# Kernel optimization log

Hardware: AMD Instinct MI355X
Metric: run time of the kernel (lower is better)

The kernel has to match this reference:

```python
import jax, jax.numpy as jnp
import numpy as np

N = 50000
E = 400000
IN_C, HID, OUT2, NCLS = 128, 512, 64, 2
NEG_SLOPE = 0.2


def setup_inputs() -> dict:
    key = jax.random.key(0)
    ks = jax.random.split(key, 12)
    x = jax.random.normal(ks[0], (N, IN_C), dtype=jnp.float32)
    edge_index = jax.random.randint(ks[1], (2, E), 0, N, dtype=jnp.int64)
    def glorot(k, shape):
        fan_in = shape[0]
        return jax.random.normal(k, shape, dtype=jnp.float32) / np.float32(np.sqrt(fan_in))
    return {
        "x": x,
        "edge_index": edge_index,
        "W1": glorot(ks[2], (IN_C, HID)),
        "a1_src": glorot(ks[3], (HID,)),
        "a1_dst": glorot(ks[4], (HID,)),
        "b1": jnp.zeros((HID,), jnp.float32),
        "W2": glorot(ks[5], (HID, OUT2)),
        "a2_src": glorot(ks[6], (OUT2,)),
        "a2_dst": glorot(ks[7], (OUT2,)),
        "b2": jnp.zeros((OUT2,), jnp.float32),
        "fcW": glorot(ks[8], (OUT2, NCLS)),
        "fcb": jnp.zeros((NCLS,), jnp.float32),
    }


def _gat_conv(h_in, src, dst, W, a_src, a_dst, b):
    # single-head GATConv (PyG defaults: heads=1, negative_slope=0.2, self-loops already added)
    h = h_in @ W                                   # [N, D]
    alpha_s = h @ a_src                            # [N]
    alpha_d = h @ a_dst                            # [N]
    e = jax.nn.leaky_relu(alpha_s[src] + alpha_d[dst], NEG_SLOPE)  # [E']
    # segment softmax over incoming edges of each dst node
    m = jax.ops.segment_max(e, dst, num_segments=N)
    ex = jnp.exp(e - m[dst])
    denom = jax.ops.segment_sum(ex, dst, num_segments=N)
    alpha = ex / denom[dst]                        # [E']
    out = jax.ops.segment_sum(alpha[:, None] * h[src], dst, num_segments=N)
    return out + b


def reference(x, edge_index, W1, a1_src, a1_dst, b1, W2, a2_src, a2_dst, b2, fcW, fcb):
    loops = jnp.arange(N, dtype=edge_index.dtype)
    src = jnp.concatenate([edge_index[0], loops])  # add self loops (PyG default)
    dst = jnp.concatenate([edge_index[1], loops])
    h = jax.nn.relu(_gat_conv(x, src, dst, W1, a1_src, a1_dst, b1))
    h = jax.nn.relu(_gat_conv(h, src, dst, W2, a2_src, a2_dst, b2))
    # F.dropout(training=self.training): identity in eval mode
    return h @ fcW + fcb
```

## Files before the change

kernel.cpp:

```cpp
#include <hip/hip_runtime.h>

#define N_NODES 50000
#define N_EDGES 400000
#define E_TOT   (N_EDGES + N_NODES)
#define IN_C 128
#define HID  512
#define OUT2 64
#define NEG_SLOPE 0.2f

typedef short bf16x8 __attribute__((ext_vector_type(8)));
typedef float f32x4  __attribute__((ext_vector_type(4)));

__device__ __forceinline__ float wave_sum(float v) {
#pragma unroll
  for (int o = 32; o > 0; o >>= 1) v += __shfl_xor(v, o, 64);
  return v;
}
__device__ __forceinline__ int wave_sum_i(int v) {
#pragma unroll
  for (int o = 32; o > 0; o >>= 1) v += __shfl_xor(v, o, 64);
  return v;
}
__device__ __forceinline__ float wave_max(float v) {
#pragma unroll
  for (int o = 32; o > 0; o >>= 1) v = fmaxf(v, __shfl_xor(v, o, 64));
  return v;
}
__device__ __forceinline__ float leaky(float t) {
  return (t > 0.f) ? t : NEG_SLOPE * t;
}

__device__ __forceinline__ unsigned short bf16_rne(float x) {
  unsigned u = __float_as_uint(x);
  u += 0x7fffu + ((u >> 16) & 1u);
  return (unsigned short)(u >> 16);
}
__device__ __forceinline__ void split_bf16(float x, unsigned short& h, unsigned short& l) {
  h = bf16_rne(x);
  float hf = __uint_as_float(((unsigned)h) << 16);
  l = bf16_rne(x - hf);
}

__device__ __forceinline__ int esrc(const int* __restrict__ ei, int e) {
  return (e < N_EDGES) ? ei[e] : (e - N_EDGES);
}
__device__ __forceinline__ int edst(const int* __restrict__ ei, int e) {
  return (e < N_EDGES) ? ei[N_EDGES + e] : (e - N_EDGES);
}

__global__ void count_deg(const int* __restrict__ ei, int* __restrict__ deg) {
  int e = blockIdx.x * blockDim.x + threadIdx.x;
  if (e >= E_TOT) return;
  atomicAdd(&deg[edst(ei, e)], 1);
}

__global__ void scanA(const int* __restrict__ deg, int* __restrict__ bsum) {
  __shared__ int ws[16];
  int t = threadIdx.x, lane = t & 63, w = t >> 6;
  int i = blockIdx.x * 1024 + t;
  int v = (i < N_NODES) ? deg[i] : 0;
  int s = wave_sum_i(v);
  if (lane == 0) ws[w] = s;
  __syncthreads();
  if (t == 0) {
    int tot = 0;
#pragma unroll
    for (int k = 0; k < 16; k++) tot += ws[k];
    bsum[blockIdx.x] = tot;
  }
}

__global__ void scanB(const int* __restrict__ bsum, int* __restrict__ boff, int nb) {
  int lane = threadIdx.x;
  int v = (lane < nb) ? bsum[lane] : 0;
  int sc = v;
#pragma unroll
  for (int off = 1; off < 64; off <<= 1) {
    int u = __shfl_up(sc, off, 64);
    if (lane >= off) sc += u;
  }
  if (lane < nb) boff[lane] = sc - v;
}

__global__ void scanC(const int* __restrict__ deg, const int* __restrict__ boff,
                      int* __restrict__ row_ptr) {
  __shared__ int ws[16];
  int t = threadIdx.x, lane = t & 63, w = t >> 6;
  int i = blockIdx.x * 1024 + t;
  int v = (i < N_NODES) ? deg[i] : 0;
  int sc = v;
#pragma unroll
  for (int off = 1; off < 64; off <<= 1) {
    int u = __shfl_up(sc, off, 64);
    if (lane >= off) sc += u;
  }
  if (lane == 63) ws[w] = sc;
  __syncthreads();
  if (w == 0 && lane < 16) {
    int u = ws[lane];
#pragma unroll
    for (int off = 1; off < 16; off <<= 1) {
      int uu = __shfl_up(u, off, 64);
      if (lane >= off) u += uu;
    }
    ws[lane] = u;
  }
  __syncthreads();
  int excl = ((w > 0) ? ws[w - 1] : 0) + boff[blockIdx.x];
  if (i < N_NODES) row_ptr[i + 1] = sc + excl;
  if (blockIdx.x == 0 && t == 0) row_ptr[0] = 0;
}

__global__ void fill_csr(const int* __restrict__ ei, const int* __restrict__ row_ptr,
                         int* __restrict__ cursor, int* __restrict__ csr_src) {
  int e = blockIdx.x * blockDim.x + threadIdx.x;
  if (e >= E_TOT) return;
  int d = edst(ei, e);
  int pos = atomicAdd(&cursor[d], 1);
  csr_src[row_ptr[d] + pos] = esrc(ei, e);
}

__global__ void prep_w1_frag(const float* __restrict__ W1, unsigned short* __restrict__ W1F) {
  int t = blockIdx.x * 256 + threadIdx.x;
  if (t >= 128 * 64) return;
  int fi = t >> 6, l = t & 63;
  int ks = fi & 3, n = (fi >> 2) & 3, jt = fi >> 4;
  int col = jt * 64 + n * 16 + (l & 15);
  int k0 = ks * 32 + (l >> 4) * 8;
  unsigned short hv[8], lv[8];
#pragma unroll
  for (int e = 0; e < 8; e++)
    split_bf16(W1[(size_t)(k0 + e) * HID + col], hv[e], lv[e]);
  unsigned short* ph = W1F + ((size_t)(fi * 2 + 0) * 64 + l) * 8;
  unsigned short* pl = W1F + ((size_t)(fi * 2 + 1) * 64 + l) * 8;
#pragma unroll
  for (int e = 0; e < 8; e++) { ph[e] = hv[e]; pl[e] = lv[e]; }
}

__global__ void prep_w2_frag(const float* __restrict__ W2, unsigned short* __restrict__ W2F) {
  int t = blockIdx.x * 256 + threadIdx.x;
  if (t >= 64 * 64) return;
  int fi = t >> 6, l = t & 63;
  int n = fi & 3, ks = (fi >> 2) & 1, jt = fi >> 3;
  int col = n * 16 + (l & 15);
  int k0 = jt * 64 + ks * 32 + (l >> 4) * 8;
  unsigned short hv[8], lv[8];
#pragma unroll
  for (int e = 0; e < 8; e++)
    split_bf16(W2[(size_t)(k0 + e) * OUT2 + col], hv[e], lv[e]);
  unsigned short* ph = W2F + ((size_t)(fi * 2 + 0) * 64 + l) * 8;
  unsigned short* pl = W2F + ((size_t)(fi * 2 + 1) * 64 + l) * 8;
#pragma unroll
  for (int e = 0; e < 8; e++) { ph[e] = hv[e]; pl[e] = lv[e]; }
}

__global__ void matvec_w1(const float* __restrict__ W1, const float* __restrict__ a1s,
                          const float* __restrict__ a1d, float* __restrict__ w1s,
                          float* __restrict__ w1d) {
  int wid = (blockIdx.x * blockDim.x + threadIdx.x) >> 6;
  int lane = threadIdx.x & 63;
  if (wid >= IN_C) return;
  const float* row = W1 + (size_t)wid * HID;
  float s = 0.f, d = 0.f;
#pragma unroll
  for (int j0 = 0; j0 < HID; j0 += 64) {
    float w = row[j0 + lane];
    s += w * a1s[j0 + lane];
    d += w * a1d[j0 + lane];
  }
  s = wave_sum(s); d = wave_sum(d);
  if (lane == 0) { w1s[wid] = s; w1d[wid] = d; }
}

__global__ void node_scores128(const float* __restrict__ x, const float* __restrict__ ws,
                               const float* __restrict__ wd, float* __restrict__ as_,
                               float* __restrict__ ad_) {
  int wid = (blockIdx.x * blockDim.x + threadIdx.x) >> 6;
  int lane = threadIdx.x & 63;
  if (wid >= N_NODES) return;
  float2 v = ((const float2*)(x + (size_t)wid * IN_C))[lane];
  float2 w1 = ((const float2*)ws)[lane];
  float2 w2 = ((const float2*)wd)[lane];
  float s = wave_sum(v.x * w1.x + v.y * w1.y);
  float d = wave_sum(v.x * w2.x + v.y * w2.y);
  if (lane == 0) { as_[wid] = s; ad_[wid] = d; }
}

__global__ void sm_agg1(const int* __restrict__ row_ptr, const int* __restrict__ csr_src,
                        const float* __restrict__ as_, const float* __restrict__ ad_,
                        const float* __restrict__ x, float* __restrict__ xa) {
  int wid = (blockIdx.x * blockDim.x + threadIdx.x) >> 6;
  int lane = threadIdx.x & 63;
  if (wid >= N_NODES) return;
  int beg = row_ptr[wid], end = row_ptr[wid + 1];
  int deg = end - beg;
  float adv = ad_[wid];
  const float2* x2 = (const float2*)x;
  float2 acc = make_float2(0.f, 0.f);
  if (deg <= 64) {
    int s = 0; float sc = -3.4e38f;
    if (lane < deg) { s = csr_src[beg + lane]; sc = leaky(as_[s] + adv); }
    float m = wave_max(sc);
    float ex = (lane < deg) ? __expf(sc - m) : 0.f;
    float sum = wave_sum(ex);
    float a = ex / sum;
    int kk = 0;
    for (; kk + 4 <= deg; kk += 4) {
      float w0 = __shfl(a, kk, 64),     w1 = __shfl(a, kk + 1, 64);
      float w2 = __shfl(a, kk + 2, 64), w3 = __shfl(a, kk + 3, 64);
      int s0 = __shfl(s, kk, 64),     s1 = __shfl(s, kk + 1, 64);
      int s2 = __shfl(s, kk + 2, 64), s3 = __shfl(s, kk + 3, 64);
      float2 r0 = x2[(size_t)s0 * 64 + lane];
      float2 r1 = x2[(size_t)s1 * 64 + lane];
      float2 r2 = x2[(size_t)s2 * 64 + lane];
      float2 r3 = x2[(size_t)s3 * 64 + lane];
      acc.x += w0 * r0.x + w1 * r1.x + w2 * r2.x + w3 * r3.x;
      acc.y += w0 * r0.y + w1 * r1.y + w2 * r2.y + w3 * r3.y;
    }
    for (; kk < deg; kk++) {
      float w = __shfl(a, kk, 64);
      int sv = __shfl(s, kk, 64);
      float2 r = x2[(size_t)sv * 64 + lane];
      acc.x += w * r.x; acc.y += w * r.y;
    }
  } else {
    float m = -3.4e38f;
    for (int k = beg + lane; k < end; k += 64)
      m = fmaxf(m, leaky(as_[csr_src[k]] + adv));
    m = wave_max(m);
    float sum = 0.f;
    for (int k = beg + lane; k < end; k += 64)
      sum += __expf(leaky(as_[csr_src[k]] + adv) - m);
    sum = wave_sum(sum);
    float inv = 1.f / sum;
    for (int k = beg; k < end; k++) {
      int sv = csr_src[k];
      float w = __expf(leaky(as_[sv] + adv) - m) * inv;
      float2 r = x2[(size_t)sv * 64 + lane];
      acc.x += w * r.x; acc.y += w * r.y;
    }
  }
  ((float2*)(xa + (size_t)wid * IN_C))[lane] = acc;
}

__launch_bounds__(128, 2)
__global__ void fused_gemm_mfma(const float* __restrict__ xa,
                                const unsigned short* __restrict__ W1F,
                                const float* __restrict__ b1,
                                const unsigned short* __restrict__ W2F,
                                const float* __restrict__ a2s, const float* __restrict__ a2d,
                                float* __restrict__ h2, float* __restrict__ as2,
                                float* __restrict__ ad2) {
  __shared__ unsigned int TS[64][64];
  int t = threadIdx.x;
  int w = t >> 6;
  int l = t & 63;
  int lr = l & 15;
  int G  = l >> 4;
  int base = blockIdx.x * 64 + w * 32;

  bf16x8 aFh[2][4], aFl[2][4];
#pragma unroll
  for (int m = 0; m < 2; m++) {
    int grow = base + m * 16 + lr;
    bool ok = (grow < N_NODES);
    const float* rp = xa + (size_t)grow * IN_C;
#pragma unroll
    for (int ks = 0; ks < 4; ks++) {
      float4 v0 = make_float4(0.f, 0.f, 0.f, 0.f), v1 = v0;
      if (ok) {
        v0 = *(const float4*)(rp + ks * 32 + G * 8);
        v1 = *(const float4*)(rp + ks * 32 + G * 8 + 4);
      }
      unsigned short h, lo;
      split_bf16(v0.x, h, lo); aFh[m][ks][0] = (short)h; aFl[m][ks][0] = (short)lo;
      split_bf16(v0.y, h, lo); aFh[m][ks][1] = (short)h; aFl[m][ks][1] = (short)lo;
      split_bf16(v0.z, h, lo); aFh[m][ks][2] = (short)h; aFl[m][ks][2] = (short)lo;
      split_bf16(v0.w, h, lo); aFh[m][ks][3] = (short)h; aFl[m][ks][3] = (short)lo;
      split_bf16(v1.x, h, lo); aFh[m][ks][4] = (short)h; aFl[m][ks][4] = (short)lo;
      split_bf16(v1.y, h, lo); aFh[m][ks][5] = (short)h; aFl[m][ks][5] = (short)lo;
      split_bf16(v1.z, h, lo); aFh[m][ks][6] = (short)h; aFl[m][ks][6] = (short)lo;
      split_bf16(v1.w, h, lo); aFh[m][ks][7] = (short)h; aFl[m][ks][7] = (short)lo;
    }
  }

  const bf16x8* W1Fv = (const bf16x8*)W1F;
  const bf16x8* W2Fv = (const bf16x8*)W2F;

  f32x4 acc2[2][4];
#pragma unroll
  for (int m = 0; m < 2; m++)
#pragma unroll
    for (int n = 0; n < 4; n++) acc2[m][n] = (f32x4){0.f, 0.f, 0.f, 0.f};

  for (int jt = 0; jt < 8; jt++) {
    f32x4 acc1[2][4];
#pragma unroll
    for (int m = 0; m < 2; m++)
#pragma unroll
      for (int n = 0; n < 4; n++) acc1[m][n] = (f32x4){0.f, 0.f, 0.f, 0.f};
#pragma unroll
    for (int ks = 0; ks < 4; ks++) {
#pragma unroll
      for (int n = 0; n < 4; n++) {
        int fi = (jt * 4 + n) * 4 + ks;
        bf16x8 b_h = W1Fv[(size_t)(fi * 2 + 0) * 64 + l];
        bf16x8 b_l = W1Fv[(size_t)(fi * 2 + 1) * 64 + l];
#pragma unroll
        for (int m = 0; m < 2; m++) {
          acc1[m][n] = __builtin_amdgcn_mfma_f32_16x16x32_bf16(aFh[m][ks], b_h, acc1[m][n], 0, 0, 0);
          acc1[m][n] = __builtin_amdgcn_mfma_f32_16x16x32_bf16(aFl[m][ks], b_h, acc1[m][n], 0, 0, 0);
          acc1[m][n] = __builtin_amdgcn_mfma_f32_16x16x32_bf16(aFh[m][ks], b_l, acc1[m][n], 0, 0, 0);
        }
      }
    }
#pragma unroll
    for (int n = 0; n < 4; n++) {
      float bv = b1[jt * 64 + n * 16 + lr];
#pragma unroll
      for (int m = 0; m < 2; m++) {
#pragma unroll
        for (int r = 0; r < 4; r++) {
          float vv = fmaxf(acc1[m][n][r] + bv, 0.f);
          unsigned short hh, ll;
          split_bf16(vv, hh, ll);
          int rowL = w * 32 + m * 16 + G * 4 + r;
          int colS = (n * 16 + lr) ^ ((rowL & 7) << 2);
          TS[rowL][colS] = (unsigned)hh | ((unsigned)ll << 16);
        }
      }
    }
#pragma unroll
    for (int ks = 0; ks < 2; ks++) {
      int kl = ks * 32 + G * 8;
      bf16x8 a2h[2], a2l[2];
#pragma unroll
      for (int m = 0; m < 2; m++) {
        int rowA = w * 32 + m * 16 + lr;
        int sw2 = (rowA & 7) << 2;
        uint4 q0 = *(const uint4*)&TS[rowA][(kl + 0) ^ sw2];
        uint4 q1 = *(const uint4*)&TS[rowA][(kl + 4) ^ sw2];
        a2h[m][0] = (short)(q0.x & 0xffff); a2l[m][0] = (short)(q0.x >> 16);
        a2h[m][1] = (short)(q0.y & 0xffff); a2l[m][1] = (short)(q0.y >> 16);
        a2h[m][2] = (short)(q0.z & 0xffff); a2l[m][2] = (short)(q0.z >> 16);
        a2h[m][3] = (short)(q0.w & 0xffff); a2l[m][3] = (short)(q0.w >> 16);
        a2h[m][4] = (short)(q1.x & 0xffff); a2l[m][4] = (short)(q1.x >> 16);
        a2h[m][5] = (short)(q1.y & 0xffff); a2l[m][5] = (short)(q1.y >> 16);
        a2h[m][6] = (short)(q1.z & 0xffff); a2l[m][6] = (short)(q1.z >> 16);
        a2h[m][7] = (short)(q1.w & 0xffff); a2l[m][7] = (short)(q1.w >> 16);
      }
#pragma unroll
      for (int n = 0; n < 4; n++) {
        int fi2 = (jt * 2 + ks) * 4 + n;
        bf16x8 b_h = W2Fv[(size_t)(fi2 * 2 + 0) * 64 + l];
        bf16x8 b_l = W2Fv[(size_t)(fi2 * 2 + 1) * 64 + l];
#pragma unroll
        for (int m = 0; m < 2; m++) {
          acc2[m][n] = __builtin_amdgcn_mfma_f32_16x16x32_bf16(a2h[m], b_h, acc2[m][n], 0, 0, 0);
          acc2[m][n] = __builtin_amdgcn_mfma_f32_16x16x32_bf16(a2l[m], b_h, acc2[m][n], 0, 0, 0);
          acc2[m][n] = __builtin_amdgcn_mfma_f32_16x16x32_bf16(a2h[m], b_l, acc2[m][n], 0, 0, 0);
        }
      }
    }
  }

#pragma unroll
  for (int m = 0; m < 2; m++) {
#pragma unroll
    for (int r = 0; r < 4; r++) {
      int grow = base + m * 16 + G * 4 + r;
      if (grow < N_NODES) {
#pragma unroll
        for (int n = 0; n < 4; n++)
          h2[(size_t)grow * OUT2 + n * 16 + lr] = acc2[m][n][r];
      }
      float sp = 0.f, dp = 0.f;
#pragma unroll
      for (int n = 0; n < 4; n++) {
        float v = acc2[m][n][r];
        sp += v * a2s[n * 16 + lr];
        dp += v * a2d[n * 16 + lr];
      }
#pragma unroll
      for (int o = 1; o < 16; o <<= 1) {
        sp += __shfl_xor(sp, o, 64);
        dp += __shfl_xor(dp, o, 64);
      }
      if (lr == 0 && grow < N_NODES) { as2[grow] = sp; ad2[grow] = dp; }
    }
  }
}

__global__ void sm_agg2_final(const int* __restrict__ row_ptr, const int* __restrict__ csr_src,
                              const float* __restrict__ as_, const float* __restrict__ ad_,
                              const float* __restrict__ h2, const float* __restrict__ b2,
                              const float* __restrict__ fcW, const float* __restrict__ fcb,
                              float* __restrict__ out) {
  int wid = (blockIdx.x * blockDim.x + threadIdx.x) >> 6;
  int lane = threadIdx.x & 63;
  if (wid >= N_NODES) return;
  int beg = row_ptr[wid], end = row_ptr[wid + 1];
  int deg = end - beg;
  float adv = ad_[wid];
  float acc = 0.f;
  if (deg <= 64) {
    int s = 0; float sc = -3.4e38f;
    if (lane < deg) { s = csr_src[beg + lane]; sc = leaky(as_[s] + adv); }
    float m = wave_max(sc);
    float ex = (lane < deg) ? __expf(sc - m) : 0.f;
    float sum = wave_sum(ex);
    float a = ex / sum;
    int kk = 0;
    for (; kk + 4 <= deg; kk += 4) {
      float w0 = __shfl(a, kk, 64),     w1 = __shfl(a, kk + 1, 64);
      float w2 = __shfl(a, kk + 2, 64), w3 = __shfl(a, kk + 3, 64);
      int s0 = __shfl(s, kk, 64),     s1 = __shfl(s, kk + 1, 64);
      int s2 = __shfl(s, kk + 2, 64), s3 = __shfl(s, kk + 3, 64);
      float r0 = h2[(size_t)s0 * OUT2 + lane];
      float r1 = h2[(size_t)s1 * OUT2 + lane];
      float r2 = h2[(size_t)s2 * OUT2 + lane];
      float r3 = h2[(size_t)s3 * OUT2 + lane];
      acc += w0 * r0 + w1 * r1 + w2 * r2 + w3 * r3;
    }
    for (; kk < deg; kk++) {
      float w = __shfl(a, kk, 64);
      int sv = __shfl(s, kk, 64);
      acc += w * h2[(size_t)sv * OUT2 + lane];
    }
  } else {
    float m = -3.4e38f;
    for (int k = beg + lane; k < end; k += 64)
      m = fmaxf(m, leaky(as_[csr_src[k]] + adv));
    m = wave_max(m);
    float sum = 0.f;
    for (int k = beg + lane; k < end; k += 64)
      sum += __expf(leaky(as_[csr_src[k]] + adv) - m);
    sum = wave_sum(sum);
    float inv = 1.f / sum;
    for (int k = beg; k < end; k++) {
      int sv = csr_src[k];
      float w = __expf(leaky(as_[sv] + adv) - m) * inv;
      acc += w * h2[(size_t)sv * OUT2 + lane];
    }
  }
  float v = fmaxf(acc + b2[lane], 0.f);
  float2 fw = ((const float2*)fcW)[lane];
  float f0 = wave_sum(v * fw.x);
  float f1 = wave_sum(v * fw.y);
  if (lane == 0) {
    out[(size_t)wid * 2 + 0] = f0 + fcb[0];
    out[(size_t)wid * 2 + 1] = f1 + fcb[1];
  }
}

extern "C" void kernel_launch(void* const* d_in, const int* in_sizes, int n_in,
                              void* d_out, int out_size, void* d_ws, size_t ws_size,
                              hipStream_t stream) {
  const float* x    = (const float*)d_in[0];
  const int*   ei   = (const int*)d_in[1];
  const float* W1   = (const float*)d_in[2];
  const float* a1s  = (const float*)d_in[3];
  const float* a1d  = (const float*)d_in[4];
  const float* b1   = (const float*)d_in[5];
  const float* W2   = (const float*)d_in[6];
  const float* a2s  = (const float*)d_in[7];
  const float* a2d  = (const float*)d_in[8];
  const float* b2   = (const float*)d_in[9];
  const float* fcW  = (const float*)d_in[10];
  const float* fcb  = (const float*)d_in[11];
  float* out = (float*)d_out;

  char* p = (char*)d_ws;
  float* xa    = (float*)p; p += (size_t)N_NODES * IN_C * 4;
  float* h2    = (float*)p; p += (size_t)N_NODES * OUT2 * 4;
  float* as1   = (float*)p; p += (size_t)N_NODES * 4;
  float* ad1   = (float*)p; p += (size_t)N_NODES * 4;
  float* w1s   = (float*)p; p += 256 * 4;
  float* w1d   = (float*)p; p += 256 * 4;
  int* row_ptr = (int*)p;   p += (size_t)(N_NODES + 4) * 4;
  int* deg     = (int*)p;   p += (size_t)N_NODES * 4;
  int* bsum    = (int*)p;   p += 64 * 4;
  int* boff    = (int*)p;   p += 64 * 4;
  int* csr_src = (int*)p;   p += (size_t)E_TOT * 4;
  unsigned short* W1F = (unsigned short*)p; p += (size_t)128 * 2 * 64 * 8 * 2;
  unsigned short* W2F = (unsigned short*)p; p += (size_t)64 * 2 * 64 * 8 * 2;

  const int edge_blocks = (E_TOT + 255) / 256;
  const int node_wave_blocks = (N_NODES + 3) / 4;
  const int m_tiles64 = (N_NODES + 63) / 64;
  const int scan_blocks = (N_NODES + 1023) / 1024;

  hipMemsetAsync(deg, 0, (size_t)N_NODES * 4, stream);
  count_deg<<<edge_blocks, 256, 0, stream>>>(ei, deg);
  scanA<<<scan_blocks, 1024, 0, stream>>>(deg, bsum);
  scanB<<<1, 64, 0, stream>>>(bsum, boff, scan_blocks);
  scanC<<<scan_blocks, 1024, 0, stream>>>(deg, boff, row_ptr);
  hipMemsetAsync(deg, 0, (size_t)N_NODES * 4, stream);
  fill_csr<<<edge_blocks, 256, 0, stream>>>(ei, row_ptr, deg, csr_src);
  prep_w1_frag<<<(128 * 64 + 255) / 256, 256, 0, stream>>>(W1, W1F);
  prep_w2_frag<<<(64 * 64 + 255) / 256, 256, 0, stream>>>(W2, W2F);

  matvec_w1<<<(IN_C + 3) / 4, 256, 0, stream>>>(W1, a1s, a1d, w1s, w1d);
  node_scores128<<<node_wave_blocks, 256, 0, stream>>>(x, w1s, w1d, as1, ad1);
  sm_agg1<<<node_wave_blocks, 256, 0, stream>>>(row_ptr, csr_src, as1, ad1, x, xa);

  fused_gemm_mfma<<<m_tiles64, 128, 0, stream>>>(xa, W1F, b1, W2F,
                                                 a2s, a2d, h2, as1, ad1);

  sm_agg2_final<<<node_wave_blocks, 256, 0, stream>>>(row_ptr, csr_src, as1, ad1, h2, b2,
                                                      fcW, fcb, out);
}
```

Measured before the change: 272.9 us.

## Merge weight prep kernels, unroll gather loops by 8, hoist MFMA B-fragment loads

Three weight-preparation kernels (W1 fragment split, W2 fragment split, W1·a matvec) are folded into one launch to cut launch overhead. The gather-aggregate loops in both softmax-aggregation kernels gain an 8-wide unrolled stage, so more independent row loads are in flight per wave. In the fused MFMA GEMM, the W1 and W2 fragment loads are batched ahead of the MFMA chains to expose memory-level parallelism. In exchange, register pressure rises, which could lower occupancy.

```diff
diff --git a/kernel.cpp b/kernel.cpp
--- a/kernel.cpp
+++ b/kernel.cpp
@@ -120,56 +120,54 @@
   csr_src[row_ptr[d] + pos] = esrc(ei, e);
 }
 
-__global__ void prep_w1_frag(const float* __restrict__ W1, unsigned short* __restrict__ W1F) {
-  int t = blockIdx.x * 256 + threadIdx.x;
-  if (t >= 128 * 64) return;
-  int fi = t >> 6, l = t & 63;
-  int ks = fi & 3, n = (fi >> 2) & 3, jt = fi >> 4;
-  int col = jt * 64 + n * 16 + (l & 15);
-  int k0 = ks * 32 + (l >> 4) * 8;
-  unsigned short hv[8], lv[8];
-#pragma unroll
-  for (int e = 0; e < 8; e++)
-    split_bf16(W1[(size_t)(k0 + e) * HID + col], hv[e], lv[e]);
-  unsigned short* ph = W1F + ((size_t)(fi * 2 + 0) * 64 + l) * 8;
-  unsigned short* pl = W1F + ((size_t)(fi * 2 + 1) * 64 + l) * 8;
-#pragma unroll
-  for (int e = 0; e < 8; e++) { ph[e] = hv[e]; pl[e] = lv[e]; }
-}
-
-__global__ void prep_w2_frag(const float* __restrict__ W2, unsigned short* __restrict__ W2F) {
-  int t = blockIdx.x * 256 + threadIdx.x;
-  if (t >= 64 * 64) return;
-  int fi = t >> 6, l = t & 63;
-  int n = fi & 3, ks = (fi >> 2) & 1, jt = fi >> 3;
-  int col = n * 16 + (l & 15);
-  int k0 = jt * 64 + ks * 32 + (l >> 4) * 8;
-  unsigned short hv[8], lv[8];
-#pragma unroll
-  for (int e = 0; e < 8; e++)
-    split_bf16(W2[(size_t)(k0 + e) * OUT2 + col], hv[e], lv[e]);
-  unsigned short* ph = W2F + ((size_t)(fi * 2 + 0) * 64 + l) * 8;
-  unsigned short* pl = W2F + ((size_t)(fi * 2 + 1) * 64 + l) * 8;
-#pragma unroll
-  for (int e = 0; e < 8; e++) { ph[e] = hv[e]; pl[e] = lv[e]; }
-}
-
-__global__ void matvec_w1(const float* __restrict__ W1, const float* __restrict__ a1s,
-                          const float* __restrict__ a1d, float* __restrict__ w1s,
-                          float* __restrict__ w1d) {
-  int wid = (blockIdx.x * blockDim.x + threadIdx.x) >> 6;
-  int lane = threadIdx.x & 63;
-  if (wid >= IN_C) return;
-  const float* row = W1 + (size_t)wid * HID;
-  float s = 0.f, d = 0.f;
-#pragma unroll
-  for (int j0 = 0; j0 < HID; j0 += 64) {
-    float w = row[j0 + lane];
-    s += w * a1s[j0 + lane];
-    d += w * a1d[j0 + lane];
-  }
-  s = wave_sum(s); d = wave_sum(d);
-  if (lane == 0) { w1s[wid] = s; w1d[wid] = d; }
+__global__ void prep_weights(const float* __restrict__ W1, const float* __restrict__ W2,
+                             const float* __restrict__ a1s, const float* __restrict__ a1d,
+                             unsigned short* __restrict__ W1F, unsigned short* __restrict__ W2F,
+                             float* __restrict__ w1s, float* __restrict__ w1d) {
+  int b = blockIdx.x;
+  if (b < 32) {
+    int t = b * 256 + threadIdx.x;
+    int fi = t >> 6, l = t & 63;
+    int ks = fi & 3, n = (fi >> 2) & 3, jt = fi >> 4;
+    int col = jt * 64 + n * 16 + (l & 15);
+    int k0 = ks * 32 + (l >> 4) * 8;
+    unsigned short hv[8], lv[8];
+#pragma unroll
+    for (int e = 0; e < 8; e++)
+      split_bf16(W1[(size_t)(k0 + e) * HID + col], hv[e], lv[e]);
+    unsigned short* ph = W1F + ((size_t)(fi * 2 + 0) * 64 + l) * 8;
+    unsigned short* pl = W1F + ((size_t)(fi * 2 + 1) * 64 + l) * 8;
+#pragma unroll
+    for (int e = 0; e < 8; e++) { ph[e] = hv[e]; pl[e] = lv[e]; }
+  } else if (b < 48) {
+    int t = (b - 32) * 256 + threadIdx.x;
+    int fi = t >> 6, l = t & 63;
+    int n = fi & 3, ks = (fi >> 2) & 1, jt = fi >> 3;
+    int col = n * 16 + (l & 15);
+    int k0 = jt * 64 + ks * 32 + (l >> 4) * 8;
+    unsigned short hv[8], lv[8];
+#pragma unroll
+    for (int e = 0; e < 8; e++)
+      split_bf16(W2[(size_t)(k0 + e) * OUT2 + col], hv[e], lv[e]);
+    unsigned short* ph = W2F + ((size_t)(fi * 2 + 0) * 64 + l) * 8;
+    unsigned short* pl = W2F + ((size_t)(fi * 2 + 1) * 64 + l) * 8;
+#pragma unroll
+    for (int e = 0; e < 8; e++) { ph[e] = hv[e]; pl[e] = lv[e]; }
+  } else {
+    int wid = ((b - 48) * 256 + threadIdx.x) >> 6;
+    int lane = threadIdx.x & 63;
+    if (wid >= IN_C) return;
+    const float* row = W1 + (size_t)wid * HID;
+    float s = 0.f, d = 0.f;
+#pragma unroll
+    for (int j0 = 0; j0 < HID; j0 += 64) {
+      float w = row[j0 + lane];
+      s += w * a1s[j0 + lane];
+      d += w * a1d[j0 + lane];
+    }
+    s = wave_sum(s); d = wave_sum(d);
+    if (lane == 0) { w1s[wid] = s; w1d[wid] = d; }
+  }
 }
 
 __global__ void node_scores128(const float* __restrict__ x, const float* __restrict__ ws,
@@ -205,6 +203,28 @@
     float sum = wave_sum(ex);
     float a = ex / sum;
     int kk = 0;
+    for (; kk + 8 <= deg; kk += 8) {
+      float w0 = __shfl(a, kk, 64),     w1 = __shfl(a, kk + 1, 64);
+      float w2 = __shfl(a, kk + 2, 64), w3 = __shfl(a, kk + 3, 64);
+      float w4 = __shfl(a, kk + 4, 64), w5 = __shfl(a, kk + 5, 64);
+      float w6 = __shfl(a, kk + 6, 64), w7 = __shfl(a, kk + 7, 64);
+      int s0 = __shfl(s, kk, 64),     s1 = __shfl(s, kk + 1, 64);
+      int s2 = __shfl(s, kk + 2, 64), s3 = __shfl(s, kk + 3, 64);
+      int s4 = __shfl(s, kk + 4, 64), s5 = __shfl(s, kk + 5, 64);
+      int s6 = __shfl(s, kk + 6, 64), s7 = __shfl(s, kk + 7, 64);
+      float2 r0 = x2[(size_t)s0 * 64 + lane];
+      float2 r1 = x2[(size_t)s1 * 64 + lane];
+      float2 r2 = x2[(size_t)s2 * 64 + lane];
+      float2 r3 = x2[(size_t)s3 * 64 + lane];
+      float2 r4 = x2[(size_t)s4 * 64 + lane];
+      float2 r5 = x2[(size_t)s5 * 64 + lane];
+      float2 r6 = x2[(size_t)s6 * 64 + lane];
+      float2 r7 = x2[(size_t)s7 * 64 + lane];
+      acc.x += w0 * r0.x + w1 * r1.x + w2 * r2.x + w3 * r3.x
+             + w4 * r4.x + w5 * r5.x + w6 * r6.x + w7 * r7.x;
+      acc.y += w0 * r0.y + w1 * r1.y + w2 * r2.y + w3 * r3.y
+             + w4 * r4.y + w5 * r5.y + w6 * r6.y + w7 * r7.y;
+    }
     for (; kk + 4 <= deg; kk += 4) {
       float w0 = __shfl(a, kk, 64),     w1 = __shfl(a, kk + 1, 64);
       float w2 = __shfl(a, kk + 2, 64), w3 = __shfl(a, kk + 3, 64);
@@ -294,6 +314,15 @@
     for (int n = 0; n < 4; n++) acc2[m][n] = (f32x4){0.f, 0.f, 0.f, 0.f};
 
   for (int jt = 0; jt < 8; jt++) {
+    bf16x8 w2h[2][4], w2l[2][4];
+#pragma unroll
+    for (int ks = 0; ks < 2; ks++)
+#pragma unroll
+      for (int n = 0; n < 4; n++) {
+        int fi2 = (jt * 2 + ks) * 4 + n;
+        w2h[ks][n] = W2Fv[(size_t)(fi2 * 2 + 0) * 64 + l];
+        w2l[ks][n] = W2Fv[(size_t)(fi2 * 2 + 1) * 64 + l];
+      }
     f32x4 acc1[2][4];
 #pragma unroll
     for (int m = 0; m < 2; m++)
@@ -301,16 +330,20 @@
       for (int n = 0; n < 4; n++) acc1[m][n] = (f32x4){0.f, 0.f, 0.f, 0.f};
 #pragma unroll
     for (int ks = 0; ks < 4; ks++) {
+      bf16x8 bh[4], bl[4];
 #pragma unroll
       for (int n = 0; n < 4; n++) {
         int fi = (jt * 4 + n) * 4 + ks;
-        bf16x8 b_h = W1Fv[(size_t)(fi * 2 + 0) * 64 + l];
-        bf16x8 b_l = W1Fv[(size_t)(fi * 2 + 1) * 64 + l];
+        bh[n] = W1Fv[(size_t)(fi * 2 + 0) * 64 + l];
+        bl[n] = W1Fv[(size_t)(fi * 2 + 1) * 64 + l];
+      }
+#pragma unroll
+      for (int n = 0; n < 4; n++) {
 #pragma unroll
         for (int m = 0; m < 2; m++) {
-          acc1[m][n] = __builtin_amdgcn_mfma_f32_16x16x32_bf16(aFh[m][ks], b_h, acc1[m][n], 0, 0, 0);
-          acc1[m][n] = __builtin_amdgcn_mfma_f32_16x16x32_bf16(aFl[m][ks], b_h, acc1[m][n], 0, 0, 0);
-          acc1[m][n] = __builtin_amdgcn_mfma_f32_16x16x32_bf16(aFh[m][ks], b_l, acc1[m][n], 0, 0, 0);
+          acc1[m][n] = __builtin_amdgcn_mfma_f32_16x16x32_bf16(aFh[m][ks], bh[n], acc1[m][n], 0, 0, 0);
+          acc1[m][n] = __builtin_amdgcn_mfma_f32_16x16x32_bf16(aFl[m][ks], bh[n], acc1[m][n], 0, 0, 0);
+          acc1[m][n] = __builtin_amdgcn_mfma_f32_16x16x32_bf16(aFh[m][ks], bl[n], acc1[m][n], 0, 0, 0);
         }
       }
     }
@@ -351,14 +384,11 @@
       }
 #pragma unroll
       for (int n = 0; n < 4; n++) {
-        int fi2 = (jt * 2 + ks) * 4 + n;
-        bf16x8 b_h = W2Fv[(size_t)(fi2 * 2 + 0) * 64 + l];
-        bf16x8 b_l = W2Fv[(size_t)(fi2 * 2 + 1) * 64 + l];
 #pragma unroll
         for (int m = 0; m < 2; m++) {
-          acc2[m][n] = __builtin_amdgcn_mfma_f32_16x16x32_bf16(a2h[m], b_h, acc2[m][n], 0, 0, 0);
-          acc2[m][n] = __builtin_amdgcn_mfma_f32_16x16x32_bf16(a2l[m], b_h, acc2[m][n], 0, 0, 0);
-          acc2[m][n] = __builtin_amdgcn_mfma_f32_16x16x32_bf16(a2h[m], b_l, acc2[m][n], 0, 0, 0);
+          acc2[m][n] = __builtin_amdgcn_mfma_f32_16x16x32_bf16(a2h[m], w2h[ks][n], acc2[m][n], 0, 0, 0);
+          acc2[m][n] = __builtin_amdgcn_mfma_f32_16x16x32_bf16(a2l[m], w2h[ks][n], acc2[m][n], 0, 0, 0);
+          acc2[m][n] = __builtin_amdgcn_mfma_f32_16x16x32_bf16(a2h[m], w2l[ks][n], acc2[m][n], 0, 0, 0);
         }
       }
     }
@@ -411,6 +441,26 @@
     float sum = wave_sum(ex);
     float a = ex / sum;
     int kk = 0;
+    for (; kk + 8 <= deg; kk += 8) {
+      float w0 = __shfl(a, kk, 64),     w1 = __shfl(a, kk + 1, 64);
+      float w2 = __shfl(a, kk + 2, 64), w3 = __shfl(a, kk + 3, 64);
+      float w4 = __shfl(a, kk + 4, 64), w5 = __shfl(a, kk + 5, 64);
+      float w6 = __shfl(a, kk + 6, 64), w7 = __shfl(a, kk + 7, 64);
+      int s0 = __shfl(s, kk, 64),     s1 = __shfl(s, kk + 1, 64);
+      int s2 = __shfl(s, kk + 2, 64), s3 = __shfl(s, kk + 3, 64);
+      int s4 = __shfl(s, kk + 4, 64), s5 = __shfl(s, kk + 5, 64);
+      int s6 = __shfl(s, kk + 6, 64), s7 = __shfl(s, kk + 7, 64);
+      float r0 = h2[(size_t)s0 * OUT2 + lane];
+      float r1 = h2[(size_t)s1 * OUT2 + lane];
+      float r2 = h2[(size_t)s2 * OUT2 + lane];
+      float r3 = h2[(size_t)s3 * OUT2 + lane];
+      float r4 = h2[(size_t)s4 * OUT2 + lane];
+      float r5 = h2[(size_t)s5 * OUT2 + lane];
+      float r6 = h2[(size_t)s6 * OUT2 + lane];
+      float r7 = h2[(size_t)s7 * OUT2 + lane];
+      acc += w0 * r0 + w1 * r1 + w2 * r2 + w3 * r3
+           + w4 * r4 + w5 * r5 + w6 * r6 + w7 * r7;
+    }
     for (; kk + 4 <= deg; kk += 4) {
       float w0 = __shfl(a, kk, 64),     w1 = __shfl(a, kk + 1, 64);
       float w2 = __shfl(a, kk + 2, 64), w3 = __shfl(a, kk + 3, 64);
@@ -497,10 +547,8 @@
   scanC<<<scan_blocks, 1024, 0, stream>>>(deg, boff, row_ptr);
   hipMemsetAsync(deg, 0, (size_t)N_NODES * 4, stream);
   fill_csr<<<edge_blocks, 256, 0, stream>>>(ei, row_ptr, deg, csr_src);
-  prep_w1_frag<<<(128 * 64 + 255) / 256, 256, 0, stream>>>(W1, W1F);
-  prep_w2_frag<<<(64 * 64 + 255) / 256, 256, 0, stream>>>(W2, W2F);
-
-  matvec_w1<<<(IN_C + 3) / 4, 256, 0, stream>>>(W1, a1s, a1d, w1s, w1d);
+  prep_weights<<<80, 256, 0, stream>>>(W1, W2, a1s, a1d, W1F, W2F, w1s, w1d);
+
   node_scores128<<<node_wave_blocks, 256, 0, stream>>>(x, w1s, w1d, as1, ad1);
   sm_agg1<<<node_wave_blocks, 256, 0, stream>>>(row_ptr, csr_src, as1, ad1, x, xa);
 
```

Result: faster. 266.9 us (-2.2%).
